# Performance work log

Hardware: AMD Instinct MI355X
Metric: run time of the kernel (lower is better)

The kernel has to match this reference:

```python
import jax, jax.numpy as jnp
import numpy as np


def setup_inputs() -> dict:
    key = jax.random.key(0)
    ks = jax.random.split(key, 7)
    B, H, W, C = 1, 128, 128, 1280
    x = jax.random.normal(ks[0], (B, H + 1, W, C), jnp.float32)  # [B, 1+H, W, C] with cls token
    v1 = jax.random.normal(ks[1], (512, 1280), jnp.float32) * 0.02  # mapping_layers2 conv1
    v2 = jax.random.normal(ks[2], (19, 512), jnp.float32) * 0.02    # mapping_layers2 conv2
    w1 = jax.random.normal(ks[3], (512, 19), jnp.float32) * 0.02    # mapping_layers conv1
    w2 = jax.random.normal(ks[4], (1280, 512), jnp.float32) * 0.02  # mapping_layers conv2
    intra = jax.random.normal(ks[5], (32, 19, 1024), jnp.float32) * 0.02  # intra_relation_matrix_layer
    inter = jax.random.normal(ks[6], (32, 19, 19), jnp.float32) * 0.02    # inter_relation_matrix
    return {"x": x, "v1": v1, "v2": v2, "w1": w1, "w2": w2,
            "intra": intra, "inter": inter, "i": 3, "B": B, "H": H, "W": W}


def reference(x, v1, v2, w1, w2, intra, inter, i, B, H, W):
    # split cls token along dim=1, then [B,H,W,C] -> [B,C,H,W]
    cls_token = x[:, :1]
    xp = jnp.transpose(x[:, 1:], (0, 3, 1, 2))  # [B,1280,H,W]

    # mapping_layers2: 1x1 conv 1280->512->19, no bias, no activation
    h = jnp.einsum('oc,bchw->bohw', v1, xp)
    x_m = jnp.einsum('oc,bchw->bohw', v2, h)  # [B,19,H,W]

    intra_m = intra[i]  # [19,1024]
    # NOTE: torch uses .view (raw reshape of channel-major memory), NOT a transpose
    x_iv = x_m.reshape(B, H * W, 19)
    aw = jnp.einsum('bnc,ck->bnk', x_iv, intra_m)  # [B,HW,1024]
    sf = jax.lax.stop_gradient(jax.nn.softmax(aw, axis=-1))  # computed under torch.no_grad
    intra_cab = jnp.einsum('bnk,ck->bnc', sf, intra_m).reshape(B, 19, H, W)

    x_iv2 = intra_cab.reshape(B, H * W, 19)  # raw reshape again
    cab = jnp.einsum('bnc,cd->bnd', x_iv2, inter[i]).reshape(B, 19, H, W)

    # mapping_layers: 1x1 conv 19->512->1280, no bias, ReLU at the end
    h2 = jnp.einsum('oc,bchw->bohw', w1, cab)
    cab_x = jax.nn.relu(jnp.einsum('oc,bchw->bohw', w2, h2))  # [B,1280,H,W]

    att = cab_x + xp
    new_x = jnp.transpose(att, (0, 2, 3, 1))  # [B,H,W,1280]
    return jnp.concatenate([cls_token, new_x], axis=1)
```

## Files before the change

### kernel.cpp

```cpp
#include <hip/hip_runtime.h>


#define OFF_M2T 25600
#define OFF_IMT 49920
#define OFF_IM2 70400
#define OFF_XM  90880
#define OFF_CAB 402176

typedef float vf4 __attribute__((ext_vector_type(4)));

__global__ __launch_bounds__(256) void prep_kernel(
    const float* __restrict__ v1, const float* __restrict__ v2,
    const float* __restrict__ w1, const float* __restrict__ w2,
    const float* __restrict__ intra, const float* __restrict__ inter,
    const int* __restrict__ ip, float* __restrict__ ws)
{
  float* m1t = ws;
  float* m2t = ws + OFF_M2T;
  float* imt = ws + OFF_IMT;
  float* im2 = ws + OFF_IM2;
  const int blk = blockIdx.x, tid = threadIdx.x;
  if (blk < 380) {
    int g = blk * 256 + tid;
    int oidx = g >> 2, part = g & 3;
    int o = oidx / 1280, j = oidx - o * 1280;
    const float* v2r = v2 + o * 512 + part * 128;
    const float* v1c = v1 + part * 128 * 1280 + j;
    float acc = 0.f;
#pragma unroll 8
    for (int c = 0; c < 128; ++c) acc = fmaf(v2r[c], v1c[c * 1280], acc);
    acc += __shfl_xor(acc, 1);
    acc += __shfl_xor(acc, 2);
    if (part == 0) {
      m1t[j * 20 + o] = acc;
      if (o == 0) m1t[j * 20 + 19] = 0.f;
    }
  } else if (blk < 760) {
    int g = (blk - 380) * 256 + tid;
    int oidx = g >> 2, part = g & 3;
    int o = oidx / 19, d = oidx - o * 19;
    const float* w2r = w2 + o * 512 + part * 128;
    const float* w1c = w1 + part * 128 * 19 + d;
    float acc = 0.f;
#pragma unroll 8
    for (int c = 0; c < 128; ++c) acc = fmaf(w2r[c], w1c[c * 19], acc);
    acc += __shfl_xor(acc, 1);
    acc += __shfl_xor(acc, 2);
    if (part == 0) m2t[d * 1280 + o] = acc;
  } else if (blk < 836) {
    int t = (blk - 760) * 256 + tid;
    int c = t >> 10, k = t & 1023;
    int iv = *ip;
    imt[k * 20 + c] = intra[(size_t)iv * 19456 + c * 1024 + k];
    if (c == 0) imt[k * 20 + 19] = 0.f;
  } else {
    int t = (blk - 836) * 256 + tid;
    int d = t >> 10, k = t & 1023;
    int iv = *ip;
    const float* ib = intra + (size_t)iv * 19456 + k;
    const float* ir = inter + (size_t)iv * 361 + d;
    float acc = 0.f;
#pragma unroll
    for (int c = 0; c < 19; ++c) acc = fmaf(ib[c * 1024], ir[c * 19], acc);
    im2[k * 20 + d] = acc;
    if (d == 0) im2[k * 20 + 19] = 0.f;
  }
}

__global__ __launch_bounds__(1024) void xm_kernel(
    const float* __restrict__ x, const float* __restrict__ m1t,
    float* __restrict__ xm, float* __restrict__ out)
{
  __shared__ float sbuf[16 * 64 * 19];
  float* xs = sbuf;
  const int blk = blockIdx.x, tid = threadIdx.x;
  if (blk < 256) {
    const int p  = tid & 63;
    const int kp = tid >> 6;
    const int kpu = __builtin_amdgcn_readfirstlane(kp);
    const int n0 = blk * 64;
    float acc[19];
#pragma unroll
    for (int o = 0; o < 19; ++o) acc[o] = 0.f;

    for (int cc = 0; cc < 10; ++cc) {
#pragma unroll
      for (int i = 0; i < 2; ++i) {
        const int f = tid + i * 1024;
        const int px = f >> 5, g = f & 31;
        const float4 v = *reinterpret_cast<const float4*>(
            x + (size_t)(n0 + px + 128) * 1280 + cc * 128 + g * 4);
        const int gp = (g + px) & 31;
        *reinterpret_cast<float4*>(xs + px * 128 + gp * 4) = v;
      }
      __syncthreads();
      const float* wrow = m1t + (cc * 128 + kpu * 8) * 20;
#pragma unroll
      for (int h = 0; h < 2; ++h) {
        const int g = kpu * 2 + h;
        const float4 xv = *reinterpret_cast<const float4*>(
            xs + p * 128 + (((g + p) & 31) << 2));
#pragma unroll
        for (int j = 0; j < 4; ++j) {
          const float* w = wrow + (h * 4 + j) * 20;
          const float xc = (&xv.x)[j];
#pragma unroll
          for (int o = 0; o < 19; ++o) acc[o] = fmaf(xc, w[o], acc[o]);
        }
      }
      __syncthreads();
    }
#pragma unroll
    for (int o = 0; o < 19; ++o) sbuf[kp * 1216 + p * 19 + o] = acc[o];
    __syncthreads();
    for (int idx = tid; idx < 1216; idx += 1024) {
      const int o = idx >> 6, pp = idx & 63;
      float s = 0.f;
#pragma unroll
      for (int q = 0; q < 16; ++q) s += sbuf[q * 1216 + pp * 19 + o];
      xm[o * 16384 + n0 + pp] = s;
    }
  } else {
    const float4* xf = reinterpret_cast<const float4*>(x);
    float4* of = reinterpret_cast<float4*>(out);
    for (int idx = (blk - 256) * 1024 + tid; idx < 40960; idx += 8 * 1024)
      of[idx] = xf[idx];
  }
}

__global__ __launch_bounds__(1024) void soft_kernel(
    const float* __restrict__ xm, const float* __restrict__ imt,
    const float* __restrict__ im2, float* __restrict__ cab)
{
  __shared__ float red[16][64][20];
  const int blk = blockIdx.x, tid = threadIdx.x;
  const int r = tid & 63, kp = tid >> 6;
  const int kpu = __builtin_amdgcn_readfirstlane(kp);
  const int n = blk * 64 + r;

  const float* xrow = xm + (size_t)n * 19;
  float xv[19];
#pragma unroll
  for (int c = 0; c < 19; ++c) xv[c] = xrow[c];
  float outp[19];
#pragma unroll
  for (int c = 0; c < 19; ++c) outp[c] = 0.f;
  float Z = 0.f;
  const int kbase = kpu * 64;
  for (int k = kbase; k < kbase + 64; ++k) {
    const float* w = imt + k * 20;
    const float* u = im2 + k * 20;
    float s0 = 0.f, s1 = 0.f, s2 = 0.f, s3 = 0.f;
#pragma unroll
    for (int c = 0; c < 16; c += 4) {
      s0 = fmaf(xv[c + 0], w[c + 0], s0);
      s1 = fmaf(xv[c + 1], w[c + 1], s1);
      s2 = fmaf(xv[c + 2], w[c + 2], s2);
      s3 = fmaf(xv[c + 3], w[c + 3], s3);
    }
    s0 = fmaf(xv[16], w[16], s0);
    s1 = fmaf(xv[17], w[17], s1);
    s2 = fmaf(xv[18], w[18], s2);
    float s = (s0 + s1) + (s2 + s3);
    float pv = __expf(s);
    Z += pv;
#pragma unroll
    for (int c = 0; c < 19; ++c) outp[c] = fmaf(pv, u[c], outp[c]);
  }
#pragma unroll
  for (int c = 0; c < 19; ++c) red[kp][r][c] = outp[c];
  red[kp][r][19] = Z;
  __syncthreads();
  for (int idx = tid; idx < 64 * 19; idx += 1024) {
    int rr = idx / 19, d = idx % 19;
    float s = 0.f, Zs = 0.f;
#pragma unroll
    for (int q = 0; q < 16; ++q) { s += red[q][rr][d]; Zs += red[q][rr][19]; }
    cab[(size_t)blk * 64 * 19 + idx] = s / Zs;
  }
}

__global__ __launch_bounds__(320, 4) void out_kernel(
    const float* __restrict__ x, const float* __restrict__ m2t,
    const float* __restrict__ cab, float* __restrict__ out)
{
  const int blk = blockIdx.x, tid = threadIdx.x;
  const int c4 = tid * 4;
  float4 mq[19];
#pragma unroll
  for (int d = 0; d < 19; ++d)
    mq[d] = *reinterpret_cast<const float4*>(m2t + d * 1280 + c4);
  const int hw0 = blk * 8;
#pragma unroll
  for (int grp = 0; grp < 2; ++grp) {
    const int p0 = grp * 4;
    float4 xv[4];
#pragma unroll
    for (int q = 0; q < 4; ++q)
      xv[q] = *reinterpret_cast<const float4*>(
          x + (size_t)(hw0 + p0 + q + 128) * 1280 + c4);
#pragma unroll
    for (int q = 0; q < 4; ++q) {
      const int p = p0 + q;
      float4 a = make_float4(0.f, 0.f, 0.f, 0.f);
#pragma unroll
      for (int d = 0; d < 19; ++d) {
        const float f = cab[d * 16384 + hw0 + p];
        a.x = fmaf(mq[d].x, f, a.x);
        a.y = fmaf(mq[d].y, f, a.y);
        a.z = fmaf(mq[d].z, f, a.z);
        a.w = fmaf(mq[d].w, f, a.w);
      }
      vf4 o4;
      o4.x = fmaxf(a.x, 0.f) + xv[q].x;
      o4.y = fmaxf(a.y, 0.f) + xv[q].y;
      o4.z = fmaxf(a.z, 0.f) + xv[q].z;
      o4.w = fmaxf(a.w, 0.f) + xv[q].w;
      const size_t addr = (size_t)(hw0 + p + 128) * 1280 + c4;
      __builtin_nontemporal_store(o4, reinterpret_cast<vf4*>(out + addr));
    }
  }
}

extern "C" void kernel_launch(void* const* d_in, const int* in_sizes, int n_in,
                              void* d_out, int out_size, void* d_ws, size_t ws_size,
                              hipStream_t stream)
{
  const float* x     = (const float*)d_in[0];
  const float* v1    = (const float*)d_in[1];
  const float* v2    = (const float*)d_in[2];
  const float* w1    = (const float*)d_in[3];
  const float* w2    = (const float*)d_in[4];
  const float* intra = (const float*)d_in[5];
  const float* inter = (const float*)d_in[6];
  const int*   ip    = (const int*)d_in[7];
  float* out = (float*)d_out;
  float* ws  = (float*)d_ws;

  prep_kernel<<<912, 256, 0, stream>>>(v1, v2, w1, w2, intra, inter, ip, ws);
  xm_kernel<<<264, 1024, 0, stream>>>(x, ws , ws + OFF_XM, out);
  soft_kernel<<<256, 1024, 0, stream>>>(ws + OFF_XM, ws + OFF_IMT, ws + OFF_IM2, ws + OFF_CAB);
  out_kernel<<<2048, 320, 0, stream>>>(x, ws + OFF_M2T, ws + OFF_CAB, out);
}
```

Baseline: 113.8 us.

## Double-buffer x tiles in xm_kernel and stage xm rows via LDS in soft_kernel

xm_kernel now double-buffers its shared-memory x tiles. It prefetches the next 128-channel chunk into registers while computing on the current one, which drops one barrier per iteration. Accumulators are held in named scalars instead of arrays. soft_kernel loads its 64 rows of xm into shared memory with coalesced reads before the main loop, rather than doing strided per-thread global loads, and it unrolls the dot products by hand. The double buffer uses more LDS, which is still within the 19456-float allocation, and more registers for the prefetched values.

```diff
diff --git a/kernel.cpp b/kernel.cpp
--- a/kernel.cpp
+++ b/kernel.cpp
@@ -67,51 +67,86 @@
   }
 }
 
+#define XM_FMA19(XC, W)                                                  \
+  a00 = fmaf((XC), (W)[0],  a00); a01 = fmaf((XC), (W)[1],  a01);        \
+  a02 = fmaf((XC), (W)[2],  a02); a03 = fmaf((XC), (W)[3],  a03);        \
+  a04 = fmaf((XC), (W)[4],  a04); a05 = fmaf((XC), (W)[5],  a05);        \
+  a06 = fmaf((XC), (W)[6],  a06); a07 = fmaf((XC), (W)[7],  a07);        \
+  a08 = fmaf((XC), (W)[8],  a08); a09 = fmaf((XC), (W)[9],  a09);        \
+  a10 = fmaf((XC), (W)[10], a10); a11 = fmaf((XC), (W)[11], a11);        \
+  a12 = fmaf((XC), (W)[12], a12); a13 = fmaf((XC), (W)[13], a13);        \
+  a14 = fmaf((XC), (W)[14], a14); a15 = fmaf((XC), (W)[15], a15);        \
+  a16 = fmaf((XC), (W)[16], a16); a17 = fmaf((XC), (W)[17], a17);        \
+  a18 = fmaf((XC), (W)[18], a18);
+
 __global__ __launch_bounds__(1024) void xm_kernel(
     const float* __restrict__ x, const float* __restrict__ m1t,
     float* __restrict__ xm, float* __restrict__ out)
 {
-  __shared__ float sbuf[16 * 64 * 19];
-  float* xs = sbuf;
+  __shared__ float sbuf[19456];
   const int blk = blockIdx.x, tid = threadIdx.x;
   if (blk < 256) {
     const int p  = tid & 63;
     const int kp = tid >> 6;
     const int kpu = __builtin_amdgcn_readfirstlane(kp);
     const int n0 = blk * 64;
-    float acc[19];
-#pragma unroll
-    for (int o = 0; o < 19; ++o) acc[o] = 0.f;
+    const float* xg = x + (size_t)(n0 + 128) * 1280;
+
+    const int px0 = tid >> 5, g0 = tid & 31;
+    const int px1 = px0 + 32;
+    const size_t ga0 = (size_t)px0 * 1280 + g0 * 4;
+    const size_t ga1 = (size_t)px1 * 1280 + g0 * 4;
+    const int st0 = px0 * 128 + (((g0 + px0) & 31) << 2);
+    const int st1 = px1 * 128 + (((g0 + px1) & 31) << 2);
+    const int rd0 = p * 128 + ((((kpu * 2 + 0) + p) & 31) << 2);
+    const int rd1 = p * 128 + ((((kpu * 2 + 1) + p) & 31) << 2);
+
+    float a00 = 0.f, a01 = 0.f, a02 = 0.f, a03 = 0.f, a04 = 0.f;
+    float a05 = 0.f, a06 = 0.f, a07 = 0.f, a08 = 0.f, a09 = 0.f;
+    float a10 = 0.f, a11 = 0.f, a12 = 0.f, a13 = 0.f, a14 = 0.f;
+    float a15 = 0.f, a16 = 0.f, a17 = 0.f, a18 = 0.f;
+
+    {
+      const float4 r0 = *reinterpret_cast<const float4*>(xg + ga0);
+      const float4 r1 = *reinterpret_cast<const float4*>(xg + ga1);
+      *reinterpret_cast<float4*>(sbuf + st0) = r0;
+      *reinterpret_cast<float4*>(sbuf + st1) = r1;
+    }
+    __syncthreads();
 
     for (int cc = 0; cc < 10; ++cc) {
-#pragma unroll
-      for (int i = 0; i < 2; ++i) {
-        const int f = tid + i * 1024;
-        const int px = f >> 5, g = f & 31;
-        const float4 v = *reinterpret_cast<const float4*>(
-            x + (size_t)(n0 + px + 128) * 1280 + cc * 128 + g * 4);
-        const int gp = (g + px) & 31;
-        *reinterpret_cast<float4*>(xs + px * 128 + gp * 4) = v;
+      float4 n0v, n1v;
+      if (cc < 9) {
+        n0v = *reinterpret_cast<const float4*>(xg + ga0 + (cc + 1) * 128);
+        n1v = *reinterpret_cast<const float4*>(xg + ga1 + (cc + 1) * 128);
+      }
+      const float* buf = sbuf + (cc & 1) * 8192;
+      const float4 xv0 = *reinterpret_cast<const float4*>(buf + rd0);
+      const float4 xv1 = *reinterpret_cast<const float4*>(buf + rd1);
+      const float* wrow = m1t + (cc * 128 + kpu * 8) * 20;
+      XM_FMA19(xv0.x, wrow);
+      XM_FMA19(xv0.y, wrow + 20);
+      XM_FMA19(xv0.z, wrow + 40);
+      XM_FMA19(xv0.w, wrow + 60);
+      XM_FMA19(xv1.x, wrow + 80);
+      XM_FMA19(xv1.y, wrow + 100);
+      XM_FMA19(xv1.z, wrow + 120);
+      XM_FMA19(xv1.w, wrow + 140);
+      if (cc < 9) {
+        float* nbuf = sbuf + ((cc + 1) & 1) * 8192;
+        *reinterpret_cast<float4*>(nbuf + st0) = n0v;
+        *reinterpret_cast<float4*>(nbuf + st1) = n1v;
       }
       __syncthreads();
-      const float* wrow = m1t + (cc * 128 + kpu * 8) * 20;
-#pragma unroll
-      for (int h = 0; h < 2; ++h) {
-        const int g = kpu * 2 + h;
-        const float4 xv = *reinterpret_cast<const float4*>(
-            xs + p * 128 + (((g + p) & 31) << 2));
-#pragma unroll
-        for (int j = 0; j < 4; ++j) {
-          const float* w = wrow + (h * 4 + j) * 20;
-          const float xc = (&xv.x)[j];
-#pragma unroll
-          for (int o = 0; o < 19; ++o) acc[o] = fmaf(xc, w[o], acc[o]);
-        }
-      }
-      __syncthreads();
-    }
-#pragma unroll
-    for (int o = 0; o < 19; ++o) sbuf[kp * 1216 + p * 19 + o] = acc[o];
+    }
+
+    {
+      float* rb = sbuf + kp * 1216 + p * 19;
+      rb[0] = a00;  rb[1] = a01;  rb[2] = a02;  rb[3] = a03;  rb[4] = a04;
+      rb[5] = a05;  rb[6] = a06;  rb[7] = a07;  rb[8] = a08;  rb[9] = a09;
+      rb[10] = a10; rb[11] = a11; rb[12] = a12; rb[13] = a13; rb[14] = a14;
+      rb[15] = a15; rb[16] = a16; rb[17] = a17; rb[18] = a18;
+    }
     __syncthreads();
     for (int idx = tid; idx < 1216; idx += 1024) {
       const int o = idx >> 6, pp = idx & 63;
@@ -128,48 +163,73 @@
   }
 }
 
+#define SOFT_ACC19(PV, U)                                                \
+  o00 = fmaf((PV), (U)[0],  o00); o01 = fmaf((PV), (U)[1],  o01);        \
+  o02 = fmaf((PV), (U)[2],  o02); o03 = fmaf((PV), (U)[3],  o03);        \
+  o04 = fmaf((PV), (U)[4],  o04); o05 = fmaf((PV), (U)[5],  o05);        \
+  o06 = fmaf((PV), (U)[6],  o06); o07 = fmaf((PV), (U)[7],  o07);        \
+  o08 = fmaf((PV), (U)[8],  o08); o09 = fmaf((PV), (U)[9],  o09);        \
+  o10 = fmaf((PV), (U)[10], o10); o11 = fmaf((PV), (U)[11], o11);        \
+  o12 = fmaf((PV), (U)[12], o12); o13 = fmaf((PV), (U)[13], o13);        \
+  o14 = fmaf((PV), (U)[14], o14); o15 = fmaf((PV), (U)[15], o15);        \
+  o16 = fmaf((PV), (U)[16], o16); o17 = fmaf((PV), (U)[17], o17);        \
+  o18 = fmaf((PV), (U)[18], o18);
+
 __global__ __launch_bounds__(1024) void soft_kernel(
     const float* __restrict__ xm, const float* __restrict__ imt,
     const float* __restrict__ im2, float* __restrict__ cab)
 {
   __shared__ float red[16][64][20];
+  __shared__ float xstage[1216];
   const int blk = blockIdx.x, tid = threadIdx.x;
   const int r = tid & 63, kp = tid >> 6;
   const int kpu = __builtin_amdgcn_readfirstlane(kp);
-  const int n = blk * 64 + r;
-
-  const float* xrow = xm + (size_t)n * 19;
-  float xv[19];
-#pragma unroll
-  for (int c = 0; c < 19; ++c) xv[c] = xrow[c];
-  float outp[19];
-#pragma unroll
-  for (int c = 0; c < 19; ++c) outp[c] = 0.f;
+  const int n0 = blk * 64;
+
+  for (int idx = tid; idx < 1216; idx += 1024)
+    xstage[idx] = xm[(size_t)n0 * 19 + idx];
+  __syncthreads();
+
+  const float* xr = xstage + r * 19;
+  const float x00 = xr[0],  x01 = xr[1],  x02 = xr[2],  x03 = xr[3];
+  const float x04 = xr[4],  x05 = xr[5],  x06 = xr[6],  x07 = xr[7];
+  const float x08 = xr[8],  x09 = xr[9],  x10 = xr[10], x11 = xr[11];
+  const float x12 = xr[12], x13 = xr[13], x14 = xr[14], x15 = xr[15];
+  const float x16 = xr[16], x17 = xr[17], x18 = xr[18];
+
+  float o00 = 0.f, o01 = 0.f, o02 = 0.f, o03 = 0.f, o04 = 0.f;
+  float o05 = 0.f, o06 = 0.f, o07 = 0.f, o08 = 0.f, o09 = 0.f;
+  float o10 = 0.f, o11 = 0.f, o12 = 0.f, o13 = 0.f, o14 = 0.f;
+  float o15 = 0.f, o16 = 0.f, o17 = 0.f, o18 = 0.f;
   float Z = 0.f;
   const int kbase = kpu * 64;
   for (int k = kbase; k < kbase + 64; ++k) {
     const float* w = imt + k * 20;
     const float* u = im2 + k * 20;
-    float s0 = 0.f, s1 = 0.f, s2 = 0.f, s3 = 0.f;
-#pragma unroll
-    for (int c = 0; c < 16; c += 4) {
-      s0 = fmaf(xv[c + 0], w[c + 0], s0);
-      s1 = fmaf(xv[c + 1], w[c + 1], s1);
-      s2 = fmaf(xv[c + 2], w[c + 2], s2);
-      s3 = fmaf(xv[c + 3], w[c + 3], s3);
-    }
-    s0 = fmaf(xv[16], w[16], s0);
-    s1 = fmaf(xv[17], w[17], s1);
-    s2 = fmaf(xv[18], w[18], s2);
-    float s = (s0 + s1) + (s2 + s3);
-    float pv = __expf(s);
+    float s0 = x00 * w[0];
+    s0 = fmaf(x04, w[4], s0); s0 = fmaf(x08, w[8],  s0);
+    s0 = fmaf(x12, w[12], s0); s0 = fmaf(x16, w[16], s0);
+    float s1 = x01 * w[1];
+    s1 = fmaf(x05, w[5], s1); s1 = fmaf(x09, w[9],  s1);
+    s1 = fmaf(x13, w[13], s1); s1 = fmaf(x17, w[17], s1);
+    float s2 = x02 * w[2];
+    s2 = fmaf(x06, w[6], s2); s2 = fmaf(x10, w[10], s2);
+    s2 = fmaf(x14, w[14], s2); s2 = fmaf(x18, w[18], s2);
+    float s3 = x03 * w[3];
+    s3 = fmaf(x07, w[7], s3); s3 = fmaf(x11, w[11], s3);
+    s3 = fmaf(x15, w[15], s3);
+    const float s = (s0 + s1) + (s2 + s3);
+    const float pv = __expf(s);
     Z += pv;
-#pragma unroll
-    for (int c = 0; c < 19; ++c) outp[c] = fmaf(pv, u[c], outp[c]);
-  }
-#pragma unroll
-  for (int c = 0; c < 19; ++c) red[kp][r][c] = outp[c];
-  red[kp][r][19] = Z;
+    SOFT_ACC19(pv, u);
+  }
+  {
+    float* rb = &red[kp][r][0];
+    rb[0] = o00;  rb[1] = o01;  rb[2] = o02;  rb[3] = o03;  rb[4] = o04;
+    rb[5] = o05;  rb[6] = o06;  rb[7] = o07;  rb[8] = o08;  rb[9] = o09;
+    rb[10] = o10; rb[11] = o11; rb[12] = o12; rb[13] = o13; rb[14] = o14;
+    rb[15] = o15; rb[16] = o16; rb[17] = o17; rb[18] = o18; rb[19] = Z;
+  }
   __syncthreads();
   for (int idx = tid; idx < 64 * 19; idx += 1024) {
     int rr = idx / 19, d = idx % 19;
```

After: 104.8 us. -7.9%, faster.
